# Kernel tuning notes

Hardware: AMD Instinct MI355X
Metric: run time of the kernel (lower is better)

The kernel has to match this reference:

```python
import jax, jax.numpy as jnp
import numpy as np

TOP_K = 8  # num_experts_per_tok


def setup_inputs() -> dict:
    key = jax.random.key(0)
    k1, k2 = jax.random.split(key)
    hidden_states = jax.random.normal(k1, (4, 4096, 2048), dtype=jnp.float32)
    weight = jax.random.normal(k2, (128, 2048), dtype=jnp.float32) * 0.02
    return {"hidden_states": hidden_states, "weight": weight}


def reference(hidden_states, weight):
    B, S, H = hidden_states.shape
    x = hidden_states.reshape(-1, H).astype(jnp.float32)        # [T, H], T = B*S
    logits = jnp.einsum("th,eh->te", x, weight.astype(jnp.float32))  # [T, E]
    scores = jax.nn.softmax(logits, axis=-1)                    # float32 softmax
    topk_weight, topk_idx = jax.lax.top_k(scores, TOP_K)        # [T, K]
    # norm_topk_prob=True: renormalize selected probabilities
    topk_weight = topk_weight / jnp.sum(topk_weight, axis=-1, keepdims=True)
    return topk_idx, topk_weight
```

## Files before the change

kernel.cpp:

```cpp
#include <hip/hip_runtime.h>
#include <math.h>

#define T_TOKENS 16384
#define HDIM     2048
#define NEXP     128
#define TOPK     8

#define BK    64
#define NCH   (HDIM / BK)

#define F16_MIN_NORM    6.1035156e-05f
#define SPLIT_SCALE     4096.0f
#define INV_SPLIT_SCALE 2.44140625e-04f

typedef __attribute__((ext_vector_type(8))) _Float16 f16x8;
typedef __attribute__((ext_vector_type(4))) float    f32x4;

__device__ __forceinline__ void f16split(float f, _Float16& hi, _Float16& lo) {
    _Float16 h = (_Float16)f;
    float back = (float)h;
    if (fabsf(f) < F16_MIN_NORM) { h = (_Float16)0.f; back = 0.f; }
    lo = (_Float16)((f - back) * SPLIT_SCALE);
    hi = h;
}

__global__ __launch_bounds__(256) void pack_w(const float* __restrict__ w,
                                              unsigned short* __restrict__ wp1,
                                              unsigned short* __restrict__ wp2) {
    int p = blockIdx.x * 256 + threadIdx.x;
    int lane = p & 63, nt = (p >> 6) & 7, kk = p >> 9;
    int col = lane & 15, quad = lane >> 4;
    const float* src = w + (size_t)(nt * 16 + col) * HDIM + kk * 32 + quad * 8;
    unsigned short h[8], l[8];
#pragma unroll
    for (int j = 0; j < 8; ++j) {
        _Float16 hh, ll;
        f16split(src[j], hh, ll);
        union { _Float16 x; unsigned short u; } ch, cl;
        ch.x = hh; cl.x = ll;
        h[j] = ch.u; l[j] = cl.u;
    }
    *(uint4*)(wp1 + (size_t)p * 8) = *(const uint4*)h;
    *(uint4*)(wp2 + (size_t)p * 8) = *(const uint4*)l;
}

__global__ __launch_bounds__(256, 2) void moe_gate(const float* __restrict__ x,
                                                   const unsigned short* __restrict__ wp1,
                                                   const unsigned short* __restrict__ wp2,
                                                   float* __restrict__ out_idx,
                                                   float* __restrict__ out_w) {
    __shared__ __align__(16) unsigned char smem[40960];
    unsigned short* a1 = (unsigned short*)smem;
    unsigned short* a2 = (unsigned short*)(smem + 4096);
    unsigned short* b1 = (unsigned short*)(smem + 8192);
    unsigned short* b2 = (unsigned short*)(smem + 24576);
    float* epil = (float*)smem;

    const int tid  = threadIdx.x;
    const int lane = tid & 63;
    const int wv   = tid >> 6;
    const int col  = lane & 15;
    const int quad = lane >> 4;
    const long tok0 = (long)blockIdx.x * 32;

    const int srow = tid >> 3, skseg = tid & 7;
    const float* xg = x + (tok0 + srow) * HDIM + skseg * 8;
    const int kk_l = skseg >> 2, quad_s = skseg & 3;
    const int adst = (((kk_l * 2 + (srow >> 4)) * 64) + quad_s * 16 + (srow & 15)) * 8;

    f32x4 acc[2][2], accc[2][2];
#pragma unroll
    for (int m = 0; m < 2; ++m)
#pragma unroll
        for (int n = 0; n < 2; ++n) { acc[m][n] = (f32x4){0,0,0,0}; accc[m][n] = (f32x4){0,0,0,0}; }

    f32x4 xv0, xv1;

    auto load_x = [&](int ch) {
        xv0 = *(const f32x4*)(xg + ch * BK);
        xv1 = *(const f32x4*)(xg + ch * BK + 4);
    };

    auto cvt_store = [&]() {
        unsigned short h[8], l[8];
#pragma unroll
        for (int j = 0; j < 8; ++j) {
            _Float16 hh, ll;
            f16split(j < 4 ? xv0[j] : xv1[j - 4], hh, ll);
            union { _Float16 x; unsigned short u; } ch_, cl_;
            ch_.x = hh; cl_.x = ll;
            h[j] = ch_.u; l[j] = cl_.u;
        }
        *(uint4*)(a1 + adst) = *(const uint4*)h;
        *(uint4*)(a2 + adst) = *(const uint4*)l;
    };

    load_x(0);
    for (int ch = 0; ch < NCH; ++ch) {
        cvt_store();
        {
            const unsigned short* s1 = wp1 + (size_t)ch * 8192;
            const unsigned short* s2 = wp2 + (size_t)ch * 8192;
#pragma unroll
            for (int i = 0; i < 4; ++i) {
                const int off = (i * 256 + tid) * 8;
                __builtin_amdgcn_global_load_lds((const __attribute__((address_space(1))) void*)(s1 + off),
                                                 (__attribute__((address_space(3))) void*)(b1 + off), 16, 0, 0);
                __builtin_amdgcn_global_load_lds((const __attribute__((address_space(1))) void*)(s2 + off),
                                                 (__attribute__((address_space(3))) void*)(b2 + off), 16, 0, 0);
            }
        }
        __syncthreads();
        if (ch + 1 < NCH) load_x(ch + 1);

#pragma unroll
        for (int kk = 0; kk < 2; ++kk) {
            f16x8 af1[2], af2[2];
#pragma unroll
            for (int m = 0; m < 2; ++m) {
                const int ao = ((kk * 2 + m) * 64 + lane) * 8;
                af1[m] = *(const f16x8*)(a1 + ao);
                af2[m] = *(const f16x8*)(a2 + ao);
            }
#pragma unroll
            for (int n = 0; n < 2; ++n) {
                const int nt = 2 * wv + n;
                const int bo = ((kk * 8 + nt) * 64 + lane) * 8;
                f16x8 bf1 = *(const f16x8*)(b1 + bo);
                f16x8 bf2 = *(const f16x8*)(b2 + bo);
#pragma unroll
                for (int m = 0; m < 2; ++m) {
                    acc[m][n]  = __builtin_amdgcn_mfma_f32_16x16x32_f16(af1[m], bf1, acc[m][n],  0, 0, 0);
                    accc[m][n] = __builtin_amdgcn_mfma_f32_16x16x32_f16(af1[m], bf2, accc[m][n], 0, 0, 0);
                    accc[m][n] = __builtin_amdgcn_mfma_f32_16x16x32_f16(af2[m], bf1, accc[m][n], 0, 0, 0);
                }
            }
        }
        __syncthreads();
    }

#pragma unroll
    for (int m = 0; m < 2; ++m)
#pragma unroll
        for (int n = 0; n < 2; ++n)
#pragma unroll
            for (int r = 0; r < 4; ++r)
                epil[(m * 16 + quad * 4 + r) * 132 + (2 * wv + n) * 16 + col] =
                    acc[m][n][r] + accc[m][n][r] * INV_SPLIT_SCALE;
    __syncthreads();

    for (int i = 0; i < 8; ++i) {
        const int t = wv * 8 + i;
        float2 p = *(const float2*)(epil + t * 132 + 2 * lane);
        float v0 = p.x, v1 = p.y;
        const int i0 = 2 * lane, i1 = 2 * lane + 1;

        float topv[TOPK];
        int topi[TOPK];
#pragma unroll
        for (int s = 0; s < TOPK; ++s) {
            float mv = (v0 >= v1) ? v0 : v1;
            int   mi = (v0 >= v1) ? i0 : i1;
#pragma unroll
            for (int off = 32; off >= 1; off >>= 1) {
                float ov = __shfl_xor(mv, off);
                int   oi = __shfl_xor(mi, off);
                if (ov > mv || (ov == mv && oi < mi)) { mv = ov; mi = oi; }
            }
            topv[s] = mv; topi[s] = mi;
            if (i0 == mi) v0 = -INFINITY;
            if (i1 == mi) v1 = -INFINITY;
        }

        const float m = topv[0];
        float sum = 0.f;
#pragma unroll
        for (int s = 0; s < TOPK; ++s) sum += expf(topv[s] - m);
        const float inv = 1.f / sum;

        float myv = topv[0]; int myi = topi[0];
#pragma unroll
        for (int s = 1; s < TOPK; ++s)
            if (lane == s) { myv = topv[s]; myi = topi[s]; }

        if (lane < TOPK) {
            long tok = tok0 + t;
            out_idx[tok * TOPK + lane] = (float)myi;
            out_w[tok * TOPK + lane]   = expf(myv - m) * inv;
        }
    }
}

extern "C" void kernel_launch(void* const* d_in, const int* in_sizes, int n_in,
                              void* d_out, int out_size, void* d_ws, size_t ws_size,
                              hipStream_t stream) {
    const float* x = (const float*)d_in[0];
    const float* w = (const float*)d_in[1];
    float* out = (float*)d_out;

    unsigned short* wp1 = (unsigned short*)d_ws;
    unsigned short* wp2 = wp1 + (size_t)NEXP * HDIM;

    pack_w<<<(64 * 8 * 64) / 256, 256, 0, stream>>>(w, wp1, wp2);
    moe_gate<<<T_TOKENS / 32, 256, 0, stream>>>(x, wp1, wp2, out, out + (size_t)T_TOKENS * TOPK);
}
```

Before: 251.4 us.

## Double-buffer weight tiles, load activations straight to registers, enlarge token tile

The gate kernel now handles 64 tokens per block with 512 threads arranged as a 4x2 wave grid. Each wave loads its activation fragment straight into registers and splits it to f16 hi/lo there, so the A operand no longer passes through LDS. The packed weight chunks are double-buffered in LDS, and the next chunk's async copy is issued before the current chunk's MFMAs, leaving one barrier per iteration. The larger tile halves weight re-reads per token. In exchange, LDS use per block grows to 64KB and register pressure is higher, which may limit occupancy.

```diff
diff --git a/kernel.cpp b/kernel.cpp
--- a/kernel.cpp
+++ b/kernel.cpp
@@ -8,6 +8,7 @@
 
 #define BK    64
 #define NCH   (HDIM / BK)
+#define TM    64
 
 #define F16_MIN_NORM    6.1035156e-05f
 #define SPLIT_SCALE     4096.0f
@@ -44,109 +45,105 @@
     *(uint4*)(wp2 + (size_t)p * 8) = *(const uint4*)l;
 }
 
-__global__ __launch_bounds__(256, 2) void moe_gate(const float* __restrict__ x,
+__global__ __launch_bounds__(512, 2) void moe_gate(const float* __restrict__ x,
                                                    const unsigned short* __restrict__ wp1,
                                                    const unsigned short* __restrict__ wp2,
                                                    float* __restrict__ out_idx,
                                                    float* __restrict__ out_w) {
-    __shared__ __align__(16) unsigned char smem[40960];
-    unsigned short* a1 = (unsigned short*)smem;
-    unsigned short* a2 = (unsigned short*)(smem + 4096);
-    unsigned short* b1 = (unsigned short*)(smem + 8192);
-    unsigned short* b2 = (unsigned short*)(smem + 24576);
-    float* epil = (float*)smem;
+    __shared__ __align__(16) unsigned short bsm[2][2][8192];
+    float* epil = (float*)bsm;
 
     const int tid  = threadIdx.x;
     const int lane = tid & 63;
     const int wv   = tid >> 6;
+    const int wm   = wv >> 1;
+    const int wn   = wv & 1;
     const int col  = lane & 15;
     const int quad = lane >> 4;
-    const long tok0 = (long)blockIdx.x * 32;
-
-    const int srow = tid >> 3, skseg = tid & 7;
-    const float* xg = x + (tok0 + srow) * HDIM + skseg * 8;
-    const int kk_l = skseg >> 2, quad_s = skseg & 3;
-    const int adst = (((kk_l * 2 + (srow >> 4)) * 64) + quad_s * 16 + (srow & 15)) * 8;
-
-    f32x4 acc[2][2], accc[2][2];
-#pragma unroll
-    for (int m = 0; m < 2; ++m)
-#pragma unroll
-        for (int n = 0; n < 2; ++n) { acc[m][n] = (f32x4){0,0,0,0}; accc[m][n] = (f32x4){0,0,0,0}; }
-
-    f32x4 xv0, xv1;
+    const long tok0 = (long)blockIdx.x * TM;
+
+    const float* xg = x + (tok0 + wm * 16 + col) * (long)HDIM + quad * 8;
+
+    f32x4 acc[4], accc[4];
+#pragma unroll
+    for (int j = 0; j < 4; ++j) { acc[j] = (f32x4){0,0,0,0}; accc[j] = (f32x4){0,0,0,0}; }
+
+    f32x4 xa0, xa1, xb0, xb1;
 
     auto load_x = [&](int ch) {
-        xv0 = *(const f32x4*)(xg + ch * BK);
-        xv1 = *(const f32x4*)(xg + ch * BK + 4);
+        const float* p = xg + ch * BK;
+        xa0 = *(const f32x4*)(p);
+        xa1 = *(const f32x4*)(p + 4);
+        xb0 = *(const f32x4*)(p + 32);
+        xb1 = *(const f32x4*)(p + 36);
     };
 
-    auto cvt_store = [&]() {
-        unsigned short h[8], l[8];
-#pragma unroll
-        for (int j = 0; j < 8; ++j) {
-            _Float16 hh, ll;
-            f16split(j < 4 ? xv0[j] : xv1[j - 4], hh, ll);
-            union { _Float16 x; unsigned short u; } ch_, cl_;
-            ch_.x = hh; cl_.x = ll;
-            h[j] = ch_.u; l[j] = cl_.u;
-        }
-        *(uint4*)(a1 + adst) = *(const uint4*)h;
-        *(uint4*)(a2 + adst) = *(const uint4*)l;
+    auto dma_b = [&](int ch, int buf) {
+        const unsigned short* s1 = wp1 + (size_t)ch * 8192;
+        const unsigned short* s2 = wp2 + (size_t)ch * 8192;
+        unsigned short* d1 = &bsm[buf][0][0];
+        unsigned short* d2 = &bsm[buf][1][0];
+#pragma unroll
+        for (int i = 0; i < 2; ++i) {
+            const int off = (i * 512 + tid) * 8;
+            __builtin_amdgcn_global_load_lds((const __attribute__((address_space(1))) void*)(s1 + off),
+                                             (__attribute__((address_space(3))) void*)(d1 + off), 16, 0, 0);
+            __builtin_amdgcn_global_load_lds((const __attribute__((address_space(1))) void*)(s2 + off),
+                                             (__attribute__((address_space(3))) void*)(d2 + off), 16, 0, 0);
+        }
     };
 
     load_x(0);
+    dma_b(0, 0);
+    __syncthreads();
+
     for (int ch = 0; ch < NCH; ++ch) {
-        cvt_store();
-        {
-            const unsigned short* s1 = wp1 + (size_t)ch * 8192;
-            const unsigned short* s2 = wp2 + (size_t)ch * 8192;
-#pragma unroll
-            for (int i = 0; i < 4; ++i) {
-                const int off = (i * 256 + tid) * 8;
-                __builtin_amdgcn_global_load_lds((const __attribute__((address_space(1))) void*)(s1 + off),
-                                                 (__attribute__((address_space(3))) void*)(b1 + off), 16, 0, 0);
-                __builtin_amdgcn_global_load_lds((const __attribute__((address_space(1))) void*)(s2 + off),
-                                                 (__attribute__((address_space(3))) void*)(b2 + off), 16, 0, 0);
+        const int p = ch & 1;
+
+        f16x8 af1[2], af2[2];
+#pragma unroll
+        for (int kk = 0; kk < 2; ++kk) {
+            f32x4 v0 = kk ? xb0 : xa0;
+            f32x4 v1 = kk ? xb1 : xa1;
+#pragma unroll
+            for (int j = 0; j < 8; ++j) {
+                float f = (j < 4) ? v0[j] : v1[j - 4];
+                _Float16 hh, ll;
+                f16split(f, hh, ll);
+                af1[kk][j] = hh;
+                af2[kk][j] = ll;
             }
         }
-        __syncthreads();
-        if (ch + 1 < NCH) load_x(ch + 1);
-
+
+        if (ch + 1 < NCH) { load_x(ch + 1); dma_b(ch + 1, p ^ 1); }
+
+        const unsigned short* b1 = &bsm[p][0][0];
+        const unsigned short* b2 = &bsm[p][1][0];
 #pragma unroll
         for (int kk = 0; kk < 2; ++kk) {
-            f16x8 af1[2], af2[2];
-#pragma unroll
-            for (int m = 0; m < 2; ++m) {
-                const int ao = ((kk * 2 + m) * 64 + lane) * 8;
-                af1[m] = *(const f16x8*)(a1 + ao);
-                af2[m] = *(const f16x8*)(a2 + ao);
-            }
-#pragma unroll
-            for (int n = 0; n < 2; ++n) {
-                const int nt = 2 * wv + n;
+#pragma unroll
+            for (int j = 0; j < 4; ++j) {
+                const int nt = wn * 4 + j;
                 const int bo = ((kk * 8 + nt) * 64 + lane) * 8;
                 f16x8 bf1 = *(const f16x8*)(b1 + bo);
                 f16x8 bf2 = *(const f16x8*)(b2 + bo);
-#pragma unroll
-                for (int m = 0; m < 2; ++m) {
-                    acc[m][n]  = __builtin_amdgcn_mfma_f32_16x16x32_f16(af1[m], bf1, acc[m][n],  0, 0, 0);
-                    accc[m][n] = __builtin_amdgcn_mfma_f32_16x16x32_f16(af1[m], bf2, accc[m][n], 0, 0, 0);
-                    accc[m][n] = __builtin_amdgcn_mfma_f32_16x16x32_f16(af2[m], bf1, accc[m][n], 0, 0, 0);
-                }
+                acc[j]  = __builtin_amdgcn_mfma_f32_16x16x32_f16(af1[kk], bf1, acc[j],  0, 0, 0);
+                accc[j] = __builtin_amdgcn_mfma_f32_16x16x32_f16(af1[kk], bf2, accc[j], 0, 0, 0);
+                accc[j] = __builtin_amdgcn_mfma_f32_16x16x32_f16(af2[kk], bf1, accc[j], 0, 0, 0);
             }
         }
+
         __syncthreads();
     }
 
 #pragma unroll
-    for (int m = 0; m < 2; ++m)
-#pragma unroll
-        for (int n = 0; n < 2; ++n)
-#pragma unroll
-            for (int r = 0; r < 4; ++r)
-                epil[(m * 16 + quad * 4 + r) * 132 + (2 * wv + n) * 16 + col] =
-                    acc[m][n][r] + accc[m][n][r] * INV_SPLIT_SCALE;
+    for (int j = 0; j < 4; ++j) {
+        const int nt = wn * 4 + j;
+#pragma unroll
+        for (int r = 0; r < 4; ++r)
+            epil[(wm * 16 + quad * 4 + r) * 132 + nt * 16 + col] =
+                acc[j][r] + accc[j][r] * INV_SPLIT_SCALE;
+    }
     __syncthreads();
 
     for (int i = 0; i < 8; ++i) {
@@ -202,5 +199,5 @@
     unsigned short* wp2 = wp1 + (size_t)NEXP * HDIM;
 
     pack_w<<<(64 * 8 * 64) / 256, 256, 0, stream>>>(w, wp1, wp2);
-    moe_gate<<<T_TOKENS / 32, 256, 0, stream>>>(x, wp1, wp2, out, out + (size_t)T_TOKENS * TOPK);
-}
+    moe_gate<<<T_TOKENS / TM, 512, 0, stream>>>(x, wp1, wp2, out, out + (size_t)T_TOKENS * TOPK);
+}
```

Result: slower. 256.7 us (+2.1%).

## Load A directly into MFMA registers and double-buffer B through registers

Applied to the files above, without the earlier changes.

The activation tile is now loaded straight from global memory in the MFMA fragment layout and split into f16 hi/lo in registers, so it no longer goes through LDS. Weight tiles are prefetched two chunks ahead into registers and written into a double-buffered LDS region, which leaves one barrier per chunk instead of two. The aim is to overlap global loads with MFMA work and cut LDS traffic and sync stalls. In exchange, register pressure rises, which could hurt occupancy under the 2-blocks-per-SM launch bound, and each wave now redoes the A split for every token row.

```diff
diff --git a/kernel.cpp b/kernel.cpp
--- a/kernel.cpp
+++ b/kernel.cpp
@@ -8,6 +8,7 @@
 
 #define BK    64
 #define NCH   (HDIM / BK)
+#define TM    32
 
 #define F16_MIN_NORM    6.1035156e-05f
 #define SPLIT_SCALE     4096.0f
@@ -44,109 +45,128 @@
     *(uint4*)(wp2 + (size_t)p * 8) = *(const uint4*)l;
 }
 
+struct Aregs { f32x4 v[8]; };
+struct Bregs { f32x4 v[8]; };
+
 __global__ __launch_bounds__(256, 2) void moe_gate(const float* __restrict__ x,
                                                    const unsigned short* __restrict__ wp1,
                                                    const unsigned short* __restrict__ wp2,
                                                    float* __restrict__ out_idx,
                                                    float* __restrict__ out_w) {
-    __shared__ __align__(16) unsigned char smem[40960];
-    unsigned short* a1 = (unsigned short*)smem;
-    unsigned short* a2 = (unsigned short*)(smem + 4096);
-    unsigned short* b1 = (unsigned short*)(smem + 8192);
-    unsigned short* b2 = (unsigned short*)(smem + 24576);
-    float* epil = (float*)smem;
+    __shared__ __align__(16) unsigned short bsm[2][2][8192];
+    float* epil = (float*)bsm;
 
     const int tid  = threadIdx.x;
     const int lane = tid & 63;
     const int wv   = tid >> 6;
     const int col  = lane & 15;
     const int quad = lane >> 4;
-    const long tok0 = (long)blockIdx.x * 32;
-
-    const int srow = tid >> 3, skseg = tid & 7;
-    const float* xg = x + (tok0 + srow) * HDIM + skseg * 8;
-    const int kk_l = skseg >> 2, quad_s = skseg & 3;
-    const int adst = (((kk_l * 2 + (srow >> 4)) * 64) + quad_s * 16 + (srow & 15)) * 8;
+    const long tok0 = (long)blockIdx.x * TM;
+
+    const float* xg = x + (tok0 + col) * (long)HDIM + quad * 8;
 
     f32x4 acc[2][2], accc[2][2];
 #pragma unroll
     for (int m = 0; m < 2; ++m)
 #pragma unroll
-        for (int n = 0; n < 2; ++n) { acc[m][n] = (f32x4){0,0,0,0}; accc[m][n] = (f32x4){0,0,0,0}; }
-
-    f32x4 xv0, xv1;
-
-    auto load_x = [&](int ch) {
-        xv0 = *(const f32x4*)(xg + ch * BK);
-        xv1 = *(const f32x4*)(xg + ch * BK + 4);
-    };
-
-    auto cvt_store = [&]() {
-        unsigned short h[8], l[8];
-#pragma unroll
-        for (int j = 0; j < 8; ++j) {
-            _Float16 hh, ll;
-            f16split(j < 4 ? xv0[j] : xv1[j - 4], hh, ll);
-            union { _Float16 x; unsigned short u; } ch_, cl_;
-            ch_.x = hh; cl_.x = ll;
-            h[j] = ch_.u; l[j] = cl_.u;
-        }
-        *(uint4*)(a1 + adst) = *(const uint4*)h;
-        *(uint4*)(a2 + adst) = *(const uint4*)l;
-    };
-
-    load_x(0);
-    for (int ch = 0; ch < NCH; ++ch) {
-        cvt_store();
-        {
-            const unsigned short* s1 = wp1 + (size_t)ch * 8192;
-            const unsigned short* s2 = wp2 + (size_t)ch * 8192;
-#pragma unroll
-            for (int i = 0; i < 4; ++i) {
-                const int off = (i * 256 + tid) * 8;
-                __builtin_amdgcn_global_load_lds((const __attribute__((address_space(1))) void*)(s1 + off),
-                                                 (__attribute__((address_space(3))) void*)(b1 + off), 16, 0, 0);
-                __builtin_amdgcn_global_load_lds((const __attribute__((address_space(1))) void*)(s2 + off),
-                                                 (__attribute__((address_space(3))) void*)(b2 + off), 16, 0, 0);
+        for (int j = 0; j < 2; ++j) { acc[m][j] = (f32x4){0,0,0,0}; accc[m][j] = (f32x4){0,0,0,0}; }
+
+    f16x8 af1[2][2], af2[2][2];
+
+    auto loadA = [&](int ch, Aregs& A) {
+#pragma unroll
+        for (int m = 0; m < 2; ++m) {
+            const float* p = xg + (size_t)m * 16 * HDIM + ch * BK;
+            A.v[m * 4 + 0] = *(const f32x4*)(p);
+            A.v[m * 4 + 1] = *(const f32x4*)(p + 4);
+            A.v[m * 4 + 2] = *(const f32x4*)(p + 32);
+            A.v[m * 4 + 3] = *(const f32x4*)(p + 36);
+        }
+    };
+    auto loadB = [&](int ch, Bregs& B) {
+#pragma unroll
+        for (int i = 0; i < 8; ++i) {
+            const unsigned short* s = (i < 4 ? wp1 : wp2) + (size_t)ch * 8192
+                                    + ((size_t)((i & 3) * 256 + tid)) * 8;
+            B.v[i] = *(const f32x4*)s;
+        }
+    };
+    auto writeB = [&](Bregs& B, unsigned short* buf) {
+#pragma unroll
+        for (int i = 0; i < 8; ++i)
+            *(f32x4*)(buf + (i >> 2) * 8192 + ((i & 3) * 256 + tid) * 8) = B.v[i];
+    };
+    auto splitA = [&](Aregs& A) {
+#pragma unroll
+        for (int m = 0; m < 2; ++m)
+#pragma unroll
+            for (int kk = 0; kk < 2; ++kk) {
+                f32x4 v0 = A.v[m * 4 + kk * 2 + 0];
+                f32x4 v1 = A.v[m * 4 + kk * 2 + 1];
+#pragma unroll
+                for (int j = 0; j < 8; ++j) {
+                    float f = (j < 4) ? v0[j] : v1[j - 4];
+                    _Float16 hh, ll;
+                    f16split(f, hh, ll);
+                    af1[kk][m][j] = hh;
+                    af2[kk][m][j] = ll;
+                }
             }
-        }
-        __syncthreads();
-        if (ch + 1 < NCH) load_x(ch + 1);
-
-#pragma unroll
-        for (int kk = 0; kk < 2; ++kk) {
-            f16x8 af1[2], af2[2];
-#pragma unroll
-            for (int m = 0; m < 2; ++m) {
-                const int ao = ((kk * 2 + m) * 64 + lane) * 8;
-                af1[m] = *(const f16x8*)(a1 + ao);
-                af2[m] = *(const f16x8*)(a2 + ao);
-            }
-#pragma unroll
-            for (int n = 0; n < 2; ++n) {
-                const int nt = 2 * wv + n;
+    };
+
+    Aregs A;
+    Bregs B0, B1;
+
+    loadA(0, A);
+    loadB(0, B0);
+    loadB(1, B1);
+    writeB(B0, &bsm[0][0][0]);
+    asm volatile("s_waitcnt lgkmcnt(0)" ::: "memory");
+    __builtin_amdgcn_s_barrier();
+
+    auto body = [&](int ch, Bregs& Bset, Bregs& Bprev,
+                    const unsigned short* bufR, unsigned short* bufW) {
+        splitA(A);
+        if (ch + 1 < NCH) loadA(ch + 1, A);
+        if (ch + 2 < NCH) loadB(ch + 2, Bset);
+
+        const unsigned short* b1 = bufR;
+        const unsigned short* b2 = bufR + 8192;
+#pragma unroll
+        for (int kk = 0; kk < 2; ++kk)
+#pragma unroll
+            for (int j = 0; j < 2; ++j) {
+                const int nt = wv * 2 + j;
                 const int bo = ((kk * 8 + nt) * 64 + lane) * 8;
                 f16x8 bf1 = *(const f16x8*)(b1 + bo);
                 f16x8 bf2 = *(const f16x8*)(b2 + bo);
 #pragma unroll
                 for (int m = 0; m < 2; ++m) {
-                    acc[m][n]  = __builtin_amdgcn_mfma_f32_16x16x32_f16(af1[m], bf1, acc[m][n],  0, 0, 0);
-                    accc[m][n] = __builtin_amdgcn_mfma_f32_16x16x32_f16(af1[m], bf2, accc[m][n], 0, 0, 0);
-                    accc[m][n] = __builtin_amdgcn_mfma_f32_16x16x32_f16(af2[m], bf1, accc[m][n], 0, 0, 0);
+                    acc[m][j]  = __builtin_amdgcn_mfma_f32_16x16x32_f16(af1[kk][m], bf1, acc[m][j],  0, 0, 0);
+                    accc[m][j] = __builtin_amdgcn_mfma_f32_16x16x32_f16(af1[kk][m], bf2, accc[m][j], 0, 0, 0);
+                    accc[m][j] = __builtin_amdgcn_mfma_f32_16x16x32_f16(af2[kk][m], bf1, accc[m][j], 0, 0, 0);
                 }
             }
-        }
-        __syncthreads();
+
+        if (ch + 1 < NCH) writeB(Bprev, bufW);
+        asm volatile("s_waitcnt lgkmcnt(0)" ::: "memory");
+        __builtin_amdgcn_s_barrier();
+    };
+
+    for (int ch = 0; ch < NCH; ch += 2) {
+        body(ch,     B0, B1, &bsm[0][0][0], &bsm[1][0][0]);
+        body(ch + 1, B1, B0, &bsm[1][0][0], &bsm[0][0][0]);
     }
+    __syncthreads();
 
 #pragma unroll
     for (int m = 0; m < 2; ++m)
 #pragma unroll
-        for (int n = 0; n < 2; ++n)
+        for (int j = 0; j < 2; ++j)
 #pragma unroll
             for (int r = 0; r < 4; ++r)
-                epil[(m * 16 + quad * 4 + r) * 132 + (2 * wv + n) * 16 + col] =
-                    acc[m][n][r] + accc[m][n][r] * INV_SPLIT_SCALE;
+                epil[(m * 16 + quad * 4 + r) * 132 + (wv * 2 + j) * 16 + col] =
+                    acc[m][j][r] + accc[m][j][r] * INV_SPLIT_SCALE;
     __syncthreads();
 
     for (int i = 0; i < 8; ++i) {
@@ -202,5 +222,5 @@
     unsigned short* wp2 = wp1 + (size_t)NEXP * HDIM;
 
     pack_w<<<(64 * 8 * 64) / 256, 256, 0, stream>>>(w, wp1, wp2);
-    moe_gate<<<T_TOKENS / 32, 256, 0, stream>>>(x, wp1, wp2, out, out + (size_t)T_TOKENS * TOPK);
-}
+    moe_gate<<<T_TOKENS / TM, 256, 0, stream>>>(x, wp1, wp2, out, out + (size_t)T_TOKENS * TOPK);
+}
```

After: 286.6 us. 14.0% more time.

## Double-buffer LDS with manual waitcnt pipelining and 64-token tiles

Applied to the files above, without the earlier changes.

Doubles the token tile per block from 32 to 64 and the block from 256 to 512 threads, arranging the eight waves as a 2x4 grid over tokens and experts. Each block now uses 96 KB of dynamic shared memory split into two LDS buffers. While the MFMA step runs on one buffer, the next chunk of split weights is staged into the other, and activations are prefetched two chunks ahead. Explicit vmcnt/lgkmcnt waits and raw s_barrier replace the two __syncthreads per chunk. The aim is to hide global-load latency and halve weight reloads per token, at the cost of one resident block per CU and fragile hand-written wait counts.

```diff
diff --git a/kernel.cpp b/kernel.cpp
--- a/kernel.cpp
+++ b/kernel.cpp
@@ -8,6 +8,7 @@
 
 #define BK    64
 #define NCH   (HDIM / BK)
+#define TM    64
 
 #define F16_MIN_NORM    6.1035156e-05f
 #define SPLIT_SCALE     4096.0f
@@ -15,6 +16,10 @@
 
 typedef __attribute__((ext_vector_type(8))) _Float16 f16x8;
 typedef __attribute__((ext_vector_type(4))) float    f32x4;
+
+#define VMWAIT(n) asm volatile("s_waitcnt vmcnt(" #n ")" ::: "memory")
+#define LGKM0()   asm volatile("s_waitcnt lgkmcnt(0)" ::: "memory")
+#define SB0()     __builtin_amdgcn_sched_barrier(0)
 
 __device__ __forceinline__ void f16split(float f, _Float16& hi, _Float16& lo) {
     _Float16 h = (_Float16)f;
@@ -44,109 +49,135 @@
     *(uint4*)(wp2 + (size_t)p * 8) = *(const uint4*)l;
 }
 
-__global__ __launch_bounds__(256, 2) void moe_gate(const float* __restrict__ x,
+__global__ __launch_bounds__(512, 2) void moe_gate(const float* __restrict__ x,
                                                    const unsigned short* __restrict__ wp1,
                                                    const unsigned short* __restrict__ wp2,
                                                    float* __restrict__ out_idx,
                                                    float* __restrict__ out_w) {
-    __shared__ __align__(16) unsigned char smem[40960];
-    unsigned short* a1 = (unsigned short*)smem;
-    unsigned short* a2 = (unsigned short*)(smem + 4096);
-    unsigned short* b1 = (unsigned short*)(smem + 8192);
-    unsigned short* b2 = (unsigned short*)(smem + 24576);
+    extern __shared__ __align__(16) unsigned char smem[];
     float* epil = (float*)smem;
 
     const int tid  = threadIdx.x;
     const int lane = tid & 63;
     const int wv   = tid >> 6;
+    const int mg   = wv >> 2;
+    const int ng   = wv & 3;
     const int col  = lane & 15;
     const int quad = lane >> 4;
-    const long tok0 = (long)blockIdx.x * 32;
+    const long tok0 = (long)blockIdx.x * TM;
 
     const int srow = tid >> 3, skseg = tid & 7;
-    const float* xg = x + (tok0 + srow) * HDIM + skseg * 8;
-    const int kk_l = skseg >> 2, quad_s = skseg & 3;
-    const int adst = (((kk_l * 2 + (srow >> 4)) * 64) + quad_s * 16 + (srow & 15)) * 8;
+    const float* xgs = x + (tok0 + srow) * (long)HDIM + skseg * 8;
+    const int adst = (((skseg >> 2) * 4 + (srow >> 4)) * 64 + (skseg & 3) * 16 + (srow & 15)) * 8;
 
     f32x4 acc[2][2], accc[2][2];
 #pragma unroll
     for (int m = 0; m < 2; ++m)
 #pragma unroll
-        for (int n = 0; n < 2; ++n) { acc[m][n] = (f32x4){0,0,0,0}; accc[m][n] = (f32x4){0,0,0,0}; }
-
-    f32x4 xv0, xv1;
-
-    auto load_x = [&](int ch) {
-        xv0 = *(const f32x4*)(xg + ch * BK);
-        xv1 = *(const f32x4*)(xg + ch * BK + 4);
-    };
-
-    auto cvt_store = [&]() {
+        for (int j = 0; j < 2; ++j) { acc[m][j] = (f32x4){0,0,0,0}; accc[m][j] = (f32x4){0,0,0,0}; }
+
+    f32x4 Av0, Av1;
+
+    auto bufp = [&](int b) -> unsigned short* { return (unsigned short*)(smem + b * 49152); };
+
+    auto loadA = [&](int ch) {
+        Av0 = *(const f32x4*)(xgs + ch * BK);
+        Av1 = *(const f32x4*)(xgs + ch * BK + 4);
+    };
+    auto splitWriteA = [&](int b) {
         unsigned short h[8], l[8];
 #pragma unroll
         for (int j = 0; j < 8; ++j) {
             _Float16 hh, ll;
-            f16split(j < 4 ? xv0[j] : xv1[j - 4], hh, ll);
+            f16split(j < 4 ? Av0[j] : Av1[j - 4], hh, ll);
             union { _Float16 x; unsigned short u; } ch_, cl_;
             ch_.x = hh; cl_.x = ll;
             h[j] = ch_.u; l[j] = cl_.u;
         }
-        *(uint4*)(a1 + adst) = *(const uint4*)h;
-        *(uint4*)(a2 + adst) = *(const uint4*)l;
-    };
-
-    load_x(0);
-    for (int ch = 0; ch < NCH; ++ch) {
-        cvt_store();
-        {
-            const unsigned short* s1 = wp1 + (size_t)ch * 8192;
-            const unsigned short* s2 = wp2 + (size_t)ch * 8192;
-#pragma unroll
-            for (int i = 0; i < 4; ++i) {
-                const int off = (i * 256 + tid) * 8;
-                __builtin_amdgcn_global_load_lds((const __attribute__((address_space(1))) void*)(s1 + off),
-                                                 (__attribute__((address_space(3))) void*)(b1 + off), 16, 0, 0);
-                __builtin_amdgcn_global_load_lds((const __attribute__((address_space(1))) void*)(s2 + off),
-                                                 (__attribute__((address_space(3))) void*)(b2 + off), 16, 0, 0);
-            }
-        }
-        __syncthreads();
-        if (ch + 1 < NCH) load_x(ch + 1);
-
+        *(uint4*)(bufp(b) + adst)        = *(const uint4*)h;
+        *(uint4*)(bufp(b) + 4096 + adst) = *(const uint4*)l;
+    };
+    auto stageB = [&](int ch, int b) {
+        const unsigned short* s1 = wp1 + (size_t)ch * 8192;
+        const unsigned short* s2 = wp2 + (size_t)ch * 8192;
+        unsigned short* d1 = bufp(b) + 8192;
+        unsigned short* d2 = bufp(b) + 16384;
+#pragma unroll
+        for (int i = 0; i < 2; ++i) {
+            const int off = (i * 512 + tid) * 8;
+            __builtin_amdgcn_global_load_lds((const __attribute__((address_space(1))) void*)(s1 + off),
+                                             (__attribute__((address_space(3))) void*)(d1 + off), 16, 0, 0);
+            __builtin_amdgcn_global_load_lds((const __attribute__((address_space(1))) void*)(s2 + off),
+                                             (__attribute__((address_space(3))) void*)(d2 + off), 16, 0, 0);
+        }
+    };
+    auto mfmaStep = [&](int b) {
+        const unsigned short* a1 = bufp(b);
+        const unsigned short* a2 = a1 + 4096;
+        const unsigned short* b1 = a1 + 8192;
+        const unsigned short* b2 = a1 + 16384;
 #pragma unroll
         for (int kk = 0; kk < 2; ++kk) {
             f16x8 af1[2], af2[2];
 #pragma unroll
             for (int m = 0; m < 2; ++m) {
-                const int ao = ((kk * 2 + m) * 64 + lane) * 8;
+                const int ao = ((kk * 4 + (mg * 2 + m)) * 64 + lane) * 8;
                 af1[m] = *(const f16x8*)(a1 + ao);
                 af2[m] = *(const f16x8*)(a2 + ao);
             }
 #pragma unroll
-            for (int n = 0; n < 2; ++n) {
-                const int nt = 2 * wv + n;
+            for (int j = 0; j < 2; ++j) {
+                const int nt = ng * 2 + j;
                 const int bo = ((kk * 8 + nt) * 64 + lane) * 8;
                 f16x8 bf1 = *(const f16x8*)(b1 + bo);
                 f16x8 bf2 = *(const f16x8*)(b2 + bo);
 #pragma unroll
                 for (int m = 0; m < 2; ++m) {
-                    acc[m][n]  = __builtin_amdgcn_mfma_f32_16x16x32_f16(af1[m], bf1, acc[m][n],  0, 0, 0);
-                    accc[m][n] = __builtin_amdgcn_mfma_f32_16x16x32_f16(af1[m], bf2, accc[m][n], 0, 0, 0);
-                    accc[m][n] = __builtin_amdgcn_mfma_f32_16x16x32_f16(af2[m], bf1, accc[m][n], 0, 0, 0);
+                    acc[m][j]  = __builtin_amdgcn_mfma_f32_16x16x32_f16(af1[m], bf1, acc[m][j],  0, 0, 0);
+                    accc[m][j] = __builtin_amdgcn_mfma_f32_16x16x32_f16(af1[m], bf2, accc[m][j], 0, 0, 0);
+                    accc[m][j] = __builtin_amdgcn_mfma_f32_16x16x32_f16(af2[m], bf1, accc[m][j], 0, 0, 0);
                 }
             }
         }
-        __syncthreads();
+    };
+
+    loadA(0);
+    stageB(0, 0);
+    SB0();
+    splitWriteA(0);
+    loadA(1);
+    SB0(); VMWAIT(2); SB0();
+    LGKM0();
+    __builtin_amdgcn_s_barrier();
+
+#define ITER(CH, P, Q, LOADNEXT, WN) do {                                   \
+        stageB((CH) + 1, Q); SB0();                                         \
+        splitWriteA(Q);                                                     \
+        if (LOADNEXT) loadA((CH) + 2);                                      \
+        mfmaStep(P);                                                        \
+        SB0(); VMWAIT(WN); SB0();                                           \
+        LGKM0();                                                            \
+        __builtin_amdgcn_s_barrier();                                       \
+    } while (0)
+
+    for (int ch = 0; ch < NCH - 2; ch += 2) {
+        ITER(ch,     0, 1, 1, 2);
+        ITER(ch + 1, 1, 0, 1, 2);
     }
+    ITER(NCH - 2, 0, 1, 0, 0);
+    mfmaStep(1);
+    __syncthreads();
+
+#undef ITER
 
 #pragma unroll
     for (int m = 0; m < 2; ++m)
 #pragma unroll
-        for (int n = 0; n < 2; ++n)
+        for (int j = 0; j < 2; ++j)
 #pragma unroll
             for (int r = 0; r < 4; ++r)
-                epil[(m * 16 + quad * 4 + r) * 132 + (2 * wv + n) * 16 + col] =
-                    acc[m][n][r] + accc[m][n][r] * INV_SPLIT_SCALE;
+                epil[((mg * 2 + m) * 16 + quad * 4 + r) * 132 + (ng * 2 + j) * 16 + col] =
+                    acc[m][j][r] + accc[m][j][r] * INV_SPLIT_SCALE;
     __syncthreads();
 
     for (int i = 0; i < 8; ++i) {
@@ -202,5 +233,6 @@
     unsigned short* wp2 = wp1 + (size_t)NEXP * HDIM;
 
     pack_w<<<(64 * 8 * 64) / 256, 256, 0, stream>>>(w, wp1, wp2);
-    moe_gate<<<T_TOKENS / 32, 256, 0, stream>>>(x, wp1, wp2, out, out + (size_t)T_TOKENS * TOPK);
-}
+    moe_gate<<<T_TOKENS / TM, 512, 98304, stream>>>(x, wp1, wp2, out,
+                                                    out + (size_t)T_TOKENS * TOPK);
+}
```

After: 243.6 us. 1.03x faster.
